# Kernel optimization log

Hardware: AMD Instinct MI355X
Metric: run time of the kernel (lower is better)

Reference implementation:

```python
import jax, jax.numpy as jnp
import numpy as np

B, N, DIM, H = 4, 2048, 1024, 16
HEAD_DIM = DIM // H
SCALE = HEAD_DIM ** -0.5


def setup_inputs() -> dict:
    key = jax.random.key(0)
    k1, k2, k3 = jax.random.split(key, 3)
    x = jax.random.normal(k1, (B, N, DIM), dtype=jnp.float32)
    w_qkv = jax.random.normal(k2, (DIM, 3 * DIM), dtype=jnp.float32) * (DIM ** -0.5)
    w_proj = jax.random.normal(k3, (DIM, DIM), dtype=jnp.float32) * (DIM ** -0.5)
    b_proj = jnp.zeros((DIM,), dtype=jnp.float32)
    return {"x": x, "w_qkv": w_qkv, "w_proj": w_proj, "b_proj": b_proj}


def reference(x, w_qkv, w_proj, b_proj):
    Bs, Ns, C = x.shape
    qkv = x @ w_qkv                       # [B, N, 3C]
    q, k, v = jnp.split(qkv, 3, axis=-1)
    # [B, N, C] -> [B, H, N, D]
    def heads(t):
        return t.reshape(Bs, Ns, H, HEAD_DIM).transpose(0, 2, 1, 3)
    q, k, v = heads(q), heads(k), heads(v)
    attn = jnp.einsum('bhnd,bhmd->bhnm', q, k) * SCALE
    attn = jax.nn.softmax(attn, axis=-1)
    out = jnp.einsum('bhnm,bhmd->bhnd', attn, v)
    out = out.transpose(0, 2, 1, 3).reshape(Bs, Ns, C)
    return out @ w_proj + b_proj
```

## Files before the change

### kernel.cpp

```cpp
#include <hip/hip_runtime.h>
#include <hip/hip_bf16.h>


typedef short bf16x8 __attribute__((ext_vector_type(8)));
typedef float f32x4  __attribute__((ext_vector_type(4)));

#define BN   4
#define SEQ  2048
#define CDIM 1024
#define NH   16
#define HD   64
#define QKVN 3072
#define MTOT 8192
#define QSCALE_LOG2E 0.18033688011112042f

static __device__ __forceinline__ unsigned short f2bf(float f){
    union { float f; unsigned int i; } v; v.f = f;
    unsigned int r = v.i + 0x7FFFu + ((v.i >> 16) & 1u);
    return (unsigned short)(r >> 16);
}

static __device__ __forceinline__ unsigned int pk2bf(float a, float b){
#if __has_builtin(__builtin_amdgcn_cvt_pk_bf16_f32)
    auto r = __builtin_amdgcn_cvt_pk_bf16_f32(a, b);
    unsigned int u; __builtin_memcpy(&u, &r, 4); return u;
#else
    return (unsigned int)f2bf(a) | ((unsigned int)f2bf(b) << 16);
#endif
}

static __device__ __forceinline__ float fast_exp2(float x){
#if __has_builtin(__builtin_amdgcn_exp2f)
    return __builtin_amdgcn_exp2f(x);
#else
    return __expf(x * 0.69314718055994531f);
#endif
}

typedef __attribute__((address_space(3))) unsigned int        as3_uint;
typedef const __attribute__((address_space(1))) unsigned int  as1_uint;
static __device__ __forceinline__ void load_lds16(
    const unsigned short* g, unsigned short* l)
{
    __builtin_amdgcn_global_load_lds((as1_uint*)g, (as3_uint*)l, 16, 0, 0);
}

__global__ __launch_bounds__(256) void convert_f32_bf16(
    const float* __restrict__ in, unsigned short* __restrict__ out)
{
    size_t i = ((size_t)blockIdx.x * 256 + threadIdx.x) * 8;
    f32x4 a = *(const f32x4*)(in + i);
    f32x4 b = *(const f32x4*)(in + i + 4);
    union { unsigned int u[4]; bf16x8 v; } o;
    o.u[0] = pk2bf(a[0], a[1]); o.u[1] = pk2bf(a[2], a[3]);
    o.u[2] = pk2bf(b[0], b[1]); o.u[3] = pk2bf(b[2], b[3]);
    *(bf16x8*)(out + i) = o.v;
}

__global__ __launch_bounds__(256) void transpose_f32_to_bf16(
    const float* __restrict__ in, unsigned short* __restrict__ out,
    int in_rs, int out_rs)
{
    __shared__ unsigned short tile[32][33];
    int c0 = blockIdx.x * 32, r0 = blockIdx.y * 32;
    int tx = threadIdx.x, ty = threadIdx.y;
    #pragma unroll
    for (int j = 0; j < 4; j++)
        tile[ty + 8*j][tx] = f2bf(in[(long long)(r0 + ty + 8*j) * in_rs + c0 + tx]);
    __syncthreads();
    #pragma unroll
    for (int j = 0; j < 4; j++)
        out[(long long)(c0 + ty + 8*j) * out_rs + r0 + tx] = tile[tx][ty + 8*j];
}

template<int MODE, int NX>
__global__ __launch_bounds__(256) void gemm_lds(
    const unsigned short* __restrict__ A,
    const unsigned short* __restrict__ BT,
    void* __restrict__ Cv,
    unsigned short* __restrict__ kvpack,
    const float* __restrict__ bias,
    int K, int Cstride)
{
    __shared__ unsigned short a_lds[128*32];
    __shared__ unsigned short b_lds[128*32];

    int tid  = threadIdx.x;
    int wave = tid >> 6, lane = tid & 63, quad = lane >> 4, l15 = lane & 15;

    int nwg = gridDim.x;
    int cpx = nwg >> 3;
    int bid = blockIdx.x;
    int swz = (bid & 7) * cpx + (bid >> 3);
    int m_blk = (swz / NX) * 128, n_blk = (swz % NX) * 128;

    const unsigned short* ag = A  + (size_t)(m_blk + (tid >> 2)) * K + (tid & 3)*8;
    const unsigned short* bg = BT + (size_t)(n_blk + (tid >> 2)) * K + (tid & 3)*8;
    const size_t row64 = (size_t)64 * K;

    unsigned short* afr = a_lds + ((wave & 1)*64 + l15)*32 + quad*8;
    unsigned short* bfr = b_lds + ((wave >> 1)*64 + l15)*32 + quad*8;

    f32x4 acc[4][4];
    #pragma unroll
    for (int i = 0; i < 4; i++)
        #pragma unroll
        for (int j = 0; j < 4; j++)
            acc[i][j] = f32x4{0.f, 0.f, 0.f, 0.f};

    for (int k0 = 0; k0 < K; k0 += 32) {
        __syncthreads();
        load_lds16(ag,         a_lds + (size_t)tid*8);
        load_lds16(ag + row64, a_lds + 2048 + (size_t)tid*8);
        load_lds16(bg,         b_lds + (size_t)tid*8);
        load_lds16(bg + row64, b_lds + 2048 + (size_t)tid*8);
        ag += 32; bg += 32;
        __syncthreads();

        bf16x8 af[4], bf[4];
        #pragma unroll
        for (int i = 0; i < 4; i++) af[i] = *(const bf16x8*)(afr + 16*i*32);
        #pragma unroll
        for (int i = 0; i < 4; i++) bf[i] = *(const bf16x8*)(bfr + 16*i*32);

        #pragma unroll
        for (int mi = 0; mi < 4; mi++)
            #pragma unroll
            for (int ni = 0; ni < 4; ni++)
                acc[mi][ni] = __builtin_amdgcn_mfma_f32_16x16x32_bf16(
                                  af[mi], bf[ni], acc[mi][ni], 0, 0, 0);
    }

    int m0 = m_blk + (wave & 1) * 64;
    int n0 = n_blk + (wave >> 1) * 64;

    if constexpr (MODE == 0) {
        float* C = (float*)Cv;
        #pragma unroll
        for (int ni = 0; ni < 4; ni++) {
            int col = n0 + 16*ni + l15;
            float bv = bias ? bias[col] : 0.f;
            #pragma unroll
            for (int mi = 0; mi < 4; mi++)
                #pragma unroll
                for (int r = 0; r < 4; r++) {
                    int row = m0 + 16*mi + quad*4 + r;
                    C[(size_t)row * Cstride + col] = acc[mi][ni][r] + bv;
                }
        }
    } else {
        unsigned short* qkvo = (unsigned short*)Cv;
        int rg = n0 >> 10;
        if (rg == 0) {
            #pragma unroll
            for (int ni = 0; ni < 4; ni++) {
                int col = n0 + 16*ni + l15;
                #pragma unroll
                for (int mi = 0; mi < 4; mi++)
                    #pragma unroll
                    for (int r = 0; r < 4; r++) {
                        int row = m0 + 16*mi + quad*4 + r;
                        qkvo[(size_t)row * Cstride + col] =
                            f2bf(acc[mi][ni][r] * QSCALE_LOG2E);
                    }
            }
        } else if (rg == 1) {
            #pragma unroll
            for (int ni = 0; ni < 4; ni++) {
                int col = n0 + 16*ni + l15 - 1024;
                int h = col >> 6, d = col & 63;
                int quadd = (d & 31) >> 3, e = d & 7, dhi = d >> 5;
                #pragma unroll
                for (int mi = 0; mi < 4; mi++)
                    #pragma unroll
                    for (int r = 0; r < 4; r++) {
                        int row = m0 + 16*mi + quad*4 + r;
                        int b = row >> 11, t = (row & 2047) >> 5, key = row & 31;
                        int tb = (key >> 2) & 1;
                        int l15a = ((key >> 3) << 2) + (key & 3);
                        size_t addr =
                            ((size_t)(((b*16 + h)*64 + t)*8 + tb*2 + dhi))*512
                            + (size_t)(quadd*16 + l15a)*8 + e;
                        kvpack[addr] = f2bf(acc[mi][ni][r]);
                    }
            }
        } else {
            #pragma unroll
            for (int ni = 0; ni < 4; ni++) {
                int col = n0 + 16*ni + l15 - 2048;
                int h = col >> 6, d = col & 63;
                int db = d >> 4, l15v = d & 15;
                #pragma unroll
                for (int mi = 0; mi < 4; mi++) {
                    int row0 = m0 + 16*mi + quad*4;
                    int b = row0 >> 11, t = (row0 & 2047) >> 5, key0 = row0 & 31;
                    int quadv = key0 >> 3, e0 = key0 & 7;
                    size_t addr =
                        ((size_t)(((b*16 + h)*64 + t)*8 + 4 + db))*512
                        + (size_t)(quadv*16 + l15v)*8 + e0;
                    union { unsigned int u[2]; unsigned long long ull; } o;
                    o.u[0] = pk2bf(acc[mi][ni][0], acc[mi][ni][1]);
                    o.u[1] = pk2bf(acc[mi][ni][2], acc[mi][ni][3]);
                    *(unsigned long long*)(kvpack + addr) = o.ull;
                }
            }
        }
    }
}


__global__ __launch_bounds__(256, 4) void attn_kernel(
    const unsigned short* __restrict__ qkv,
    const unsigned short* __restrict__ kvpack,
    unsigned short* __restrict__ ctx)
{
    __shared__ unsigned short kvtile[4][4096];

    int tid  = threadIdx.x;
    int wave = tid >> 6, lane = tid & 63, quad = lane >> 4, l15 = lane & 15;
    int p  = blockIdx.x;
    int L  = (p & 7) * 128 + (p >> 3);
    int bh = L >> 4;
    int rb = L & 15;
    int b = bh >> 4, h = bh & 15;
    int i0 = rb * 128 + wave * 32;

    const unsigned short* qbA =
        qkv + (size_t)(b*SEQ + i0 + l15) * QKVN + h*HD + quad*8;
    const unsigned short* qbB = qbA + (size_t)16 * QKVN;
    bf16x8 qA0 = *(const bf16x8*)(qbA);
    bf16x8 qA1 = *(const bf16x8*)(qbA + 32);
    bf16x8 qB0 = *(const bf16x8*)(qbB);
    bf16x8 qB1 = *(const bf16x8*)(qbB + 32);

    const unsigned short* kvg = kvpack + (size_t)bh * 64 * 4096;

#define STAGE(BUF, T) do {                                                     \
        load_lds16(kvg + (size_t)(T)*4096 + tid*8,        &kvtile[BUF][tid*8]);\
        load_lds16(kvg + (size_t)(T)*4096 + 2048 + tid*8,                      \
                   &kvtile[BUF][2048 + tid*8]);                                \
    } while (0)

#define SYNC(N) do {                                                           \
        __builtin_amdgcn_sched_barrier(0);                                     \
        asm volatile("s_waitcnt vmcnt(" #N ")" ::: "memory");                  \
        __builtin_amdgcn_s_barrier();                                          \
        __builtin_amdgcn_sched_barrier(0);                                     \
    } while (0)

    const f32x4 zf = {0.f, 0.f, 0.f, 0.f};
    f32x4 oA0 = zf, oA1 = zf, oA2 = zf, oA3 = zf;
    f32x4 oB0 = zf, oB1 = zf, oB2 = zf, oB3 = zf;
    f32x4 lA = zf, lB = zf;

    bf16x8 ones;
    #pragma unroll
    for (int e = 0; e < 8; e++) ones[e] = (short)0x3F80;

#define ATTN_TILE(LK)                                                              \
    {                                                                              \
        bf16x8 k0a = *(const bf16x8*)((LK));                                       \
        bf16x8 k0b = *(const bf16x8*)((LK) + 512);                                 \
        bf16x8 k1a = *(const bf16x8*)((LK) + 1024);                                \
        bf16x8 k1b = *(const bf16x8*)((LK) + 1536);                                \
        bf16x8 v0  = *(const bf16x8*)((LK) + 2048);                                \
        bf16x8 v1  = *(const bf16x8*)((LK) + 2560);                                \
        bf16x8 v2  = *(const bf16x8*)((LK) + 3072);                                \
        bf16x8 v3  = *(const bf16x8*)((LK) + 3584);                                \
        f32x4 sA0 = __builtin_amdgcn_mfma_f32_16x16x32_bf16(k0a, qA0, zf, 0,0,0);  \
        sA0 = __builtin_amdgcn_mfma_f32_16x16x32_bf16(k0b, qA1, sA0, 0,0,0);       \
        f32x4 sA1 = __builtin_amdgcn_mfma_f32_16x16x32_bf16(k1a, qA0, zf, 0,0,0);  \
        sA1 = __builtin_amdgcn_mfma_f32_16x16x32_bf16(k1b, qA1, sA1, 0,0,0);       \
        f32x4 sB0 = __builtin_amdgcn_mfma_f32_16x16x32_bf16(k0a, qB0, zf, 0,0,0);  \
        sB0 = __builtin_amdgcn_mfma_f32_16x16x32_bf16(k0b, qB1, sB0, 0,0,0);       \
        f32x4 sB1 = __builtin_amdgcn_mfma_f32_16x16x32_bf16(k1a, qB0, zf, 0,0,0);  \
        sB1 = __builtin_amdgcn_mfma_f32_16x16x32_bf16(k1b, qB1, sB1, 0,0,0);       \
        union { unsigned int u[4]; bf16x8 v; } pkA, pkB;                           \
        pkA.u[0] = pk2bf(fast_exp2(sA0[0]), fast_exp2(sA0[1]));                    \
        pkA.u[1] = pk2bf(fast_exp2(sA0[2]), fast_exp2(sA0[3]));                    \
        pkA.u[2] = pk2bf(fast_exp2(sA1[0]), fast_exp2(sA1[1]));                    \
        pkA.u[3] = pk2bf(fast_exp2(sA1[2]), fast_exp2(sA1[3]));                    \
        pkB.u[0] = pk2bf(fast_exp2(sB0[0]), fast_exp2(sB0[1]));                    \
        pkB.u[1] = pk2bf(fast_exp2(sB0[2]), fast_exp2(sB0[3]));                    \
        pkB.u[2] = pk2bf(fast_exp2(sB1[0]), fast_exp2(sB1[1]));                    \
        pkB.u[3] = pk2bf(fast_exp2(sB1[2]), fast_exp2(sB1[3]));                    \
        lA  = __builtin_amdgcn_mfma_f32_16x16x32_bf16(pkA.v, ones, lA, 0,0,0);     \
        lB  = __builtin_amdgcn_mfma_f32_16x16x32_bf16(pkB.v, ones, lB, 0,0,0);     \
        oA0 = __builtin_amdgcn_mfma_f32_16x16x32_bf16(pkA.v, v0, oA0, 0,0,0);      \
        oA1 = __builtin_amdgcn_mfma_f32_16x16x32_bf16(pkA.v, v1, oA1, 0,0,0);      \
        oA2 = __builtin_amdgcn_mfma_f32_16x16x32_bf16(pkA.v, v2, oA2, 0,0,0);      \
        oA3 = __builtin_amdgcn_mfma_f32_16x16x32_bf16(pkA.v, v3, oA3, 0,0,0);      \
        oB0 = __builtin_amdgcn_mfma_f32_16x16x32_bf16(pkB.v, v0, oB0, 0,0,0);      \
        oB1 = __builtin_amdgcn_mfma_f32_16x16x32_bf16(pkB.v, v1, oB1, 0,0,0);      \
        oB2 = __builtin_amdgcn_mfma_f32_16x16x32_bf16(pkB.v, v2, oB2, 0,0,0);      \
        oB3 = __builtin_amdgcn_mfma_f32_16x16x32_bf16(pkB.v, v3, oB3, 0,0,0);      \
    }

    asm volatile("s_waitcnt vmcnt(0)" ::: "memory");

    STAGE(0, 0); STAGE(1, 1); STAGE(2, 2);

    const unsigned short* lds0 = &kvtile[0][lane*8];

    for (int t = 0; t < 61; ++t) {
        SYNC(4);
        STAGE((t + 3) & 3, t + 3);
        ATTN_TILE(lds0 + (t & 3) * 4096);
    }
    SYNC(4); ATTN_TILE(lds0 + 1 * 4096);
    SYNC(2); ATTN_TILE(lds0 + 2 * 4096);
    SYNC(0); ATTN_TILE(lds0 + 3 * 4096);

    #pragma unroll
    for (int r = 0; r < 4; r++) {
        float invA = 1.f / lA[r];
        float invB = 1.f / lB[r];
        int rowA = b*SEQ + i0 + quad*4 + r;
        size_t baseA = (size_t)rowA * CDIM + h*HD + l15;
        size_t baseB = baseA + (size_t)16 * CDIM;
        ctx[baseA]      = f2bf(oA0[r] * invA);
        ctx[baseA + 16] = f2bf(oA1[r] * invA);
        ctx[baseA + 32] = f2bf(oA2[r] * invA);
        ctx[baseA + 48] = f2bf(oA3[r] * invA);
        ctx[baseB]      = f2bf(oB0[r] * invB);
        ctx[baseB + 16] = f2bf(oB1[r] * invB);
        ctx[baseB + 32] = f2bf(oB2[r] * invB);
        ctx[baseB + 48] = f2bf(oB3[r] * invB);
    }
#undef STAGE
#undef SYNC
#undef ATTN_TILE
}

extern "C" void kernel_launch(void* const* d_in, const int* in_sizes, int n_in,
                              void* d_out, int out_size, void* d_ws, size_t ws_size,
                              hipStream_t stream)
{
    const float* x      = (const float*)d_in[0];
    const float* w_qkv  = (const float*)d_in[1];
    const float* w_proj = (const float*)d_in[2];
    const float* b_proj = (const float*)d_in[3];
    float* out = (float*)d_out;

    char* ws = (char*)d_ws;
    unsigned short* qkv    = (unsigned short*)(ws);
    unsigned short* ctx    = (unsigned short*)(ws + 50331648);
    unsigned short* xb     = ctx;
    unsigned short* kvpack = (unsigned short*)(ws + 67108864);
    unsigned short* wqkvT  = (unsigned short*)(ws + 100663296);
    unsigned short* wprojT = (unsigned short*)(ws + 106954752);

    dim3 tb(32, 8);
    transpose_f32_to_bf16<<<dim3(QKVN/32, CDIM/32), tb, 0, stream>>>(
        w_qkv, wqkvT, QKVN, CDIM);
    transpose_f32_to_bf16<<<dim3(CDIM/32, CDIM/32), tb, 0, stream>>>(
        w_proj, wprojT, CDIM, CDIM);

    convert_f32_bf16<<<dim3(MTOT*CDIM/2048), 256, 0, stream>>>(x, xb);

    gemm_lds<1, QKVN/128><<<dim3((QKVN/128)*(MTOT/128)), 256, 0, stream>>>(
        xb, wqkvT, qkv, kvpack, nullptr, CDIM, QKVN);

    attn_kernel<<<dim3(BN * NH * (SEQ/128)), 256, 0, stream>>>(
        qkv, kvpack, ctx);

    gemm_lds<0, CDIM/128><<<dim3((CDIM/128)*(MTOT/128)), 256, 0, stream>>>(
        ctx, wprojT, out, nullptr, b_proj, CDIM, CDIM);
}
```

Measured before the change: 276.6 us.

## Triple-buffer GEMM LDS tiles with async global-to-LDS prefetch

Replaces the single-buffered GEMM main loop, which loaded a K-tile and then waited on it before computing, with a three-stage ring of LDS buffers. Tiles for two steps ahead are issued with global_load_lds, and each iteration waits only on the older loads before running the MFMAs. This overlaps global memory latency with matrix math in the QKV and projection GEMMs. It triples LDS use per block (48KB), which may lower occupancy. The SYNC macro is moved to file scope so both kernels can share it.

Measured after the change: 275.8 us. About the same (-0.3%).

```diff
diff --git a/kernel.cpp b/kernel.cpp
--- a/kernel.cpp
+++ b/kernel.cpp
@@ -45,6 +45,13 @@
     __builtin_amdgcn_global_load_lds((as1_uint*)g, (as3_uint*)l, 16, 0, 0);
 }
 
+#define SYNC(N) do {                                                           \
+        __builtin_amdgcn_sched_barrier(0);                                     \
+        asm volatile("s_waitcnt vmcnt(" #N ")" ::: "memory");                  \
+        __builtin_amdgcn_s_barrier();                                          \
+        __builtin_amdgcn_sched_barrier(0);                                     \
+    } while (0)
+
 __global__ __launch_bounds__(256) void convert_f32_bf16(
     const float* __restrict__ in, unsigned short* __restrict__ out)
 {
@@ -82,8 +89,8 @@
     const float* __restrict__ bias,
     int K, int Cstride)
 {
-    __shared__ unsigned short a_lds[128*32];
-    __shared__ unsigned short b_lds[128*32];
+    __shared__ unsigned short a_lds[3][4096];
+    __shared__ unsigned short b_lds[3][4096];
 
     int tid  = threadIdx.x;
     int wave = tid >> 6, lane = tid & 63, quad = lane >> 4, l15 = lane & 15;
@@ -98,8 +105,17 @@
     const unsigned short* bg = BT + (size_t)(n_blk + (tid >> 2)) * K + (tid & 3)*8;
     const size_t row64 = (size_t)64 * K;
 
-    unsigned short* afr = a_lds + ((wave & 1)*64 + l15)*32 + quad*8;
-    unsigned short* bfr = b_lds + ((wave >> 1)*64 + l15)*32 + quad*8;
+#define GSTAGE(BUF, T) do {                                                    \
+        const unsigned short* ag_ = ag + (size_t)(T)*32;                       \
+        const unsigned short* bg_ = bg + (size_t)(T)*32;                       \
+        load_lds16(ag_,         &a_lds[BUF][tid*8]);                           \
+        load_lds16(ag_ + row64, &a_lds[BUF][2048 + tid*8]);                    \
+        load_lds16(bg_,         &b_lds[BUF][tid*8]);                           \
+        load_lds16(bg_ + row64, &b_lds[BUF][2048 + tid*8]);                    \
+    } while (0)
+
+    const unsigned short* afr = &a_lds[0][((wave & 1)*64 + l15)*32 + quad*8];
+    const unsigned short* bfr = &b_lds[0][((wave >> 1)*64 + l15)*32 + quad*8];
 
     f32x4 acc[4][4];
     #pragma unroll
@@ -108,28 +124,39 @@
         for (int j = 0; j < 4; j++)
             acc[i][j] = f32x4{0.f, 0.f, 0.f, 0.f};
 
-    for (int k0 = 0; k0 < K; k0 += 32) {
-        __syncthreads();
-        load_lds16(ag,         a_lds + (size_t)tid*8);
-        load_lds16(ag + row64, a_lds + 2048 + (size_t)tid*8);
-        load_lds16(bg,         b_lds + (size_t)tid*8);
-        load_lds16(bg + row64, b_lds + 2048 + (size_t)tid*8);
-        ag += 32; bg += 32;
-        __syncthreads();
-
-        bf16x8 af[4], bf[4];
-        #pragma unroll
-        for (int i = 0; i < 4; i++) af[i] = *(const bf16x8*)(afr + 16*i*32);
-        #pragma unroll
-        for (int i = 0; i < 4; i++) bf[i] = *(const bf16x8*)(bfr + 16*i*32);
+    int nk = K >> 5;
+    GSTAGE(0, 0);
+    GSTAGE(1, 1);
+
+    int buf = 0, nbuf = 2;
+    for (int t = 0; t < nk; ++t) {
+        if (t + 2 < nk) {
+            SYNC(4);
+            GSTAGE(nbuf, t + 2);
+        } else if (t + 1 < nk) {
+            SYNC(4);
+        } else {
+            SYNC(0);
+        }
+
+        int bo = buf * 4096;
+        bf16x8 af[4], bfv[4];
+        #pragma unroll
+        for (int i = 0; i < 4; i++) af[i]  = *(const bf16x8*)(afr + bo + 16*i*32);
+        #pragma unroll
+        for (int i = 0; i < 4; i++) bfv[i] = *(const bf16x8*)(bfr + bo + 16*i*32);
 
         #pragma unroll
         for (int mi = 0; mi < 4; mi++)
             #pragma unroll
             for (int ni = 0; ni < 4; ni++)
                 acc[mi][ni] = __builtin_amdgcn_mfma_f32_16x16x32_bf16(
-                                  af[mi], bf[ni], acc[mi][ni], 0, 0, 0);
-    }
+                                  af[mi], bfv[ni], acc[mi][ni], 0, 0, 0);
+
+        buf  = (buf  == 2) ? 0 : buf  + 1;
+        nbuf = (nbuf == 2) ? 0 : nbuf + 1;
+    }
+#undef GSTAGE
 
     int m0 = m_blk + (wave & 1) * 64;
     int n0 = n_blk + (wave >> 1) * 64;
@@ -239,13 +266,6 @@
         load_lds16(kvg + (size_t)(T)*4096 + tid*8,        &kvtile[BUF][tid*8]);\
         load_lds16(kvg + (size_t)(T)*4096 + 2048 + tid*8,                      \
                    &kvtile[BUF][2048 + tid*8]);                                \
-    } while (0)
-
-#define SYNC(N) do {                                                           \
-        __builtin_amdgcn_sched_barrier(0);                                     \
-        asm volatile("s_waitcnt vmcnt(" #N ")" ::: "memory");                  \
-        __builtin_amdgcn_s_barrier();                                          \
-        __builtin_amdgcn_sched_barrier(0);                                     \
     } while (0)
 
     const f32x4 zf = {0.f, 0.f, 0.f, 0.f};
@@ -328,7 +348,6 @@
         ctx[baseB + 48] = f2bf(oB3[r] * invB);
     }
 #undef STAGE
-#undef SYNC
 #undef ATTN_TILE
 }
 
```
